# Kernel tuning notes

Hardware: AMD Instinct MI355X
Metric: run time of the kernel (lower is better)

## Reference

```python
import jax, jax.numpy as jnp
import numpy as np

WS = 4            # window_size
C = 192           # dim
NH = 6            # num_heads
HD = C // NH      # head_dim
HID = 384         # mlp hidden = int(dim * mlp_ratio)
EPS = 1e-5


def _rel_pos_index(ws):
    coords = np.stack(np.meshgrid(np.arange(ws), np.arange(ws), np.arange(ws), indexing='ij'))  # [3,ws,ws,ws]
    cf = coords.reshape(3, -1)                                # [3, N]
    rel = cf[:, :, None] - cf[:, None, :]                     # [3, N, N]
    rel = rel.transpose(1, 2, 0)                              # [N, N, 3]
    rel += ws - 1
    rel[:, :, 0] *= (2 * ws - 1) * (2 * ws - 1)
    rel[:, :, 1] *= 2 * ws - 1
    return jnp.asarray(rel.sum(-1), dtype=jnp.int32)          # [N, N]

REL_IDX = _rel_pos_index(WS)


def setup_inputs() -> dict:
    key = jax.random.key(0)
    ks = jax.random.split(key, 20)
    s = 0.02
    B, Dd, Hh, Ww = 2, 48, 48, 48
    L = Dd * Hh * Ww
    tbl = (2 * WS - 1) ** 3
    return {
        'x': jax.random.normal(ks[0], (B, L, C), jnp.float32),
        'D': Dd, 'H': Hh, 'W': Ww,
        'ln1_g': jnp.ones((C,), jnp.float32), 'ln1_b': jnp.zeros((C,), jnp.float32),
        'ln2_g': jnp.ones((C,), jnp.float32), 'ln2_b': jnp.zeros((C,), jnp.float32),
        'qkv_w': jax.random.normal(ks[1], (C, 3 * C), jnp.float32) * s,
        'qkv_b': jnp.zeros((3 * C,), jnp.float32),
        'rpb_table': jax.random.normal(ks[2], (tbl, NH), jnp.float32) * s,
        'proj_w': jax.random.normal(ks[3], (C, C), jnp.float32) * s,
        'proj_b': jnp.zeros((C,), jnp.float32),
        'fc1_w': jax.random.normal(ks[4], (C, HID), jnp.float32) * s,
        'fc1_b': jnp.zeros((HID,), jnp.float32),
        'dw_w': jax.random.normal(ks[5], (HID, 1, 3, 3, 3), jnp.float32) * s,
        'dw_b': jnp.zeros((HID,), jnp.float32),
        'bn_g': jnp.ones((HID,), jnp.float32), 'bn_b': jnp.zeros((HID,), jnp.float32),
        'bn_mean': jnp.zeros((HID,), jnp.float32), 'bn_var': jnp.ones((HID,), jnp.float32),
        'fc2_w': jax.random.normal(ks[6], (HID, C), jnp.float32) * s,
        'fc2_b': jnp.zeros((C,), jnp.float32),
    }


def _ln(x, g, b):
    m = jnp.mean(x, -1, keepdims=True)
    v = jnp.mean((x - m) ** 2, -1, keepdims=True)
    return (x - m) * jax.lax.rsqrt(v + EPS) * g + b


def _window_attn(xw, qkv_w, qkv_b, rpb_table, proj_w, proj_b):
    # xw: [nW, N, C]
    nW, N, _ = xw.shape
    qkv = (xw @ qkv_w + qkv_b).reshape(nW, N, 3, NH, HD)
    q, k, v = qkv[:, :, 0], qkv[:, :, 1], qkv[:, :, 2]   # [nW, N, NH, HD]
    scale = HD ** -0.5
    attn = jnp.einsum('wnhd,wmhd->whnm', q * scale, k)    # [nW, NH, N, N]
    bias = rpb_table[REL_IDX]                              # [N, N, NH]
    attn = attn + jnp.transpose(bias, (2, 0, 1))[None]
    attn = jax.nn.softmax(attn, axis=-1)
    out = jnp.einsum('whnm,wmhd->wnhd', attn, v).reshape(nW, N, C)
    return out @ proj_w + proj_b


def reference(x, D, H, W, ln1_g, ln1_b, ln2_g, ln2_b, qkv_w, qkv_b, rpb_table,
              proj_w, proj_b, fc1_w, fc1_b, dw_w, dw_b, bn_g, bn_b, bn_mean,
              bn_var, fc2_w, fc2_b):
    B, L, _ = x.shape
    shortcut = x
    # --- windowed attention ---
    xs = _ln(x, ln1_g, ln1_b).reshape(B, D, H, W, C)
    # D,H,W divisible by WS -> no padding
    xs = xs.reshape(B, D // WS, WS, H // WS, WS, W // WS, WS, C)
    xw = jnp.transpose(xs, (0, 1, 3, 5, 2, 4, 6, 7)).reshape(-1, WS ** 3, C)
    aw = _window_attn(xw, qkv_w, qkv_b, rpb_table, proj_w, proj_b)
    aw = aw.reshape(B, D // WS, H // WS, W // WS, WS, WS, WS, C)
    xr = jnp.transpose(aw, (0, 1, 4, 2, 5, 3, 6, 7)).reshape(B, L, C)
    x = shortcut + xr
    # --- efficient MLP: fc1 -> dwconv3d -> BN(eval) -> GELU -> fc2 ---
    y = _ln(x, ln2_g, ln2_b)
    h = y @ fc1_w + fc1_b                                  # [B, L, HID]
    hs = jnp.transpose(h, (0, 2, 1)).reshape(B, HID, D, H, W)
    hs = jax.lax.conv_general_dilated(
        hs, dw_w, window_strides=(1, 1, 1), padding='SAME',
        feature_group_count=HID,
        dimension_numbers=('NCDHW', 'OIDHW', 'NCDHW')) + dw_b[None, :, None, None, None]
    hs = (hs - bn_mean[None, :, None, None, None]) * jax.lax.rsqrt(
        bn_var[None, :, None, None, None] + EPS) * bn_g[None, :, None, None, None] + bn_b[None, :, None, None, None]
    h = jnp.transpose(hs.reshape(B, HID, L), (0, 2, 1))
    h = jax.nn.gelu(h, approximate=False)
    return x + (h @ fc2_w + fc2_b)
```

## Files before the change

kernel.cpp:

```cpp
#include <hip/hip_runtime.h>

typedef __bf16 bf16;
typedef __bf16 bf16x8 __attribute__((ext_vector_type(8)));
typedef float f32x4 __attribute__((ext_vector_type(4)));

#define L_TOT 110592
#define TOKS  221184
#define NWIN  3456

static __device__ __forceinline__ f32x4 mfma16(bf16x8 a, bf16x8 b, f32x4 c) {
    return __builtin_amdgcn_mfma_f32_16x16x32_bf16(a, b, c, 0, 0, 0);
}
static __device__ __forceinline__ bf16x8 ld8(const bf16* p) { return *(const bf16x8*)p; }

__global__ void wt_frag(const float* __restrict__ src, bf16* __restrict__ dst, int K, int N) {
    int i = blockIdx.x * 256 + threadIdx.x;
    if (i >= K * N) return;
    int kw = i & 31, col = (i >> 5) & 63, rest = i >> 11;
    int nks = K >> 5;
    int ks = rest % nks, chunk = rest / nks;
    int n = chunk * 64 + col, k = ks * 32 + kw;
    dst[i] = (bf16)src[k * N + n];
}

__global__ void bias6_build(const float* __restrict__ rpb, float* __restrict__ bias6) {
    int i = blockIdx.x * 256 + threadIdx.x;
    if (i >= 6 * 64 * 64) return;
    int h = i >> 12, n = (i >> 6) & 63, m = i & 63;
    int r0 = (n >> 4) - (m >> 4) + 3;
    int r1 = ((n >> 2) & 3) - ((m >> 2) & 3) + 3;
    int r2 = (n & 3) - (m & 3) + 3;
    bias6[i] = rpb[(r0 * 49 + r1 * 7 + r2) * 6 + h];
}

__global__ void ln1_window(const float* __restrict__ x, const float* __restrict__ g,
                           const float* __restrict__ bt, bf16* __restrict__ xw) {
    int wave = threadIdx.x >> 6, lane = threadIdx.x & 63;
    int t = blockIdx.x * 4 + wave;
    const float* row = x + (long)t * 192;
    float v0 = row[lane], v1 = row[lane + 64], v2 = row[lane + 128];
    float s = v0 + v1 + v2;
    #pragma unroll
    for (int m = 1; m < 64; m <<= 1) s += __shfl_xor(s, m);
    float mu = s * (1.0f / 192.0f);
    float d0 = v0 - mu, d1 = v1 - mu, d2 = v2 - mu;
    float q = d0 * d0 + d1 * d1 + d2 * d2;
    #pragma unroll
    for (int m = 1; m < 64; m <<= 1) q += __shfl_xor(q, m);
    float r = rsqrtf(q * (1.0f / 192.0f) + 1e-5f);
    int b = t / L_TOT, l = t - b * L_TOT;
    int dz = l / 2304, rem = l - dz * 2304;
    int hy = rem / 48, wx = rem - hy * 48;
    int w = ((b * 12 + (dz >> 2)) * 12 + (hy >> 2)) * 12 + (wx >> 2);
    int n = (dz & 3) * 16 + (hy & 3) * 4 + (wx & 3);
    bf16* o = xw + (long)w * 12288 + (lane >> 5) * 2048 + n * 32 + (lane & 31);
    o[0]    = (bf16)(d0 * r * g[lane]       + bt[lane]);
    o[4096] = (bf16)(d1 * r * g[lane + 64]  + bt[lane + 64]);
    o[8192] = (bf16)(d2 * r * g[lane + 128] + bt[lane + 128]);
}

__global__ void ln2_kernel(const bf16* __restrict__ in, const float* __restrict__ g,
                           const float* __restrict__ bt, bf16* __restrict__ y) {
    int wave = threadIdx.x >> 6, lane = threadIdx.x & 63;
    long t = blockIdx.x * 4 + wave;
    const bf16* row = in + t * 192;
    float v0 = (float)row[lane], v1 = (float)row[lane + 64], v2 = (float)row[lane + 128];
    float s = v0 + v1 + v2;
    #pragma unroll
    for (int m = 1; m < 64; m <<= 1) s += __shfl_xor(s, m);
    float mu = s * (1.0f / 192.0f);
    float d0 = v0 - mu, d1 = v1 - mu, d2 = v2 - mu;
    float q = d0 * d0 + d1 * d1 + d2 * d2;
    #pragma unroll
    for (int m = 1; m < 64; m <<= 1) q += __shfl_xor(q, m);
    float r = rsqrtf(q * (1.0f / 192.0f) + 1e-5f);
    bf16* o = y + (t >> 6) * 12288 + (lane >> 5) * 2048 + (t & 63) * 32 + (lane & 31);
    o[0]    = (bf16)(d0 * r * g[lane]       + bt[lane]);
    o[4096] = (bf16)(d1 * r * g[lane + 64]  + bt[lane + 64]);
    o[8192] = (bf16)(d2 * r * g[lane + 128] + bt[lane + 128]);
}

__global__ __launch_bounds__(256) void gemm_qkv(
    const bf16* __restrict__ xw, const bf16* __restrict__ wt,
    const float* __restrict__ bqkv,
    bf16* __restrict__ qb, bf16* __restrict__ kb_, bf16* __restrict__ vtb) {
    int m0 = blockIdx.x * 128;
    int w0 = m0 >> 6;
    int wid = threadIdx.x >> 6, lane = threadIdx.x & 63;
    int wr = wid >> 1, wc = wid & 1;
    int lo = lane & 15, hi = lane >> 4;
    f32x4 zf = {0.f, 0.f, 0.f, 0.f};

    const bf16* Ab = xw + (long)(w0 + wr) * 12288 + (lo * 32 + hi * 8);
    bf16x8 a[4][6];
    #pragma unroll
    for (int ti = 0; ti < 4; ++ti)
        #pragma unroll
        for (int ks = 0; ks < 6; ++ks)
            a[ti][ks] = ld8(Ab + ks * 2048 + ti * 512);

    #pragma unroll
    for (int nc = 0; nc < 9; ++nc) {
        int sect = nc / 3;
        int cb0 = (nc - sect * 3) * 64;
        f32x4 acc[4][2];
        #pragma unroll
        for (int i = 0; i < 4; ++i) { acc[i][0] = zf; acc[i][1] = zf; }
        const bf16* Bb = wt + (long)nc * 12288 + (wc * 32 + lo) * 32 + hi * 8;
        #pragma unroll
        for (int ks = 0; ks < 6; ++ks) {
            bf16x8 b0 = ld8(Bb + ks * 2048);
            bf16x8 b1 = ld8(Bb + ks * 2048 + 512);
            #pragma unroll
            for (int ti = 0; ti < 4; ++ti) {
                acc[ti][0] = mfma16(a[ti][ks], b0, acc[ti][0]);
                acc[ti][1] = mfma16(a[ti][ks], b1, acc[ti][1]);
            }
        }
        #pragma unroll
        for (int ti = 0; ti < 4; ++ti)
            #pragma unroll
            for (int j = 0; j < 4; ++j) {
                int trow = m0 + wr * 64 + ti * 16 + hi * 4 + j;
                int w = trow >> 6, n = trow & 63;
                #pragma unroll
                for (int tj = 0; tj < 2; ++tj) {
                    int cw = cb0 + wc * 32 + tj * 16 + lo;
                    int h = cw >> 5, d = cw & 31;
                    float val = acc[ti][tj][j] + bqkv[sect * 192 + cw];
                    long wh = (long)(w * 6 + h);
                    if (sect == 0)       qb[(wh * 64 + n) * 32 + d] = (bf16)(val * 0.17677669529663687f);
                    else if (sect == 1)  kb_[(wh * 64 + n) * 32 + d] = (bf16)val;
                    else                 vtb[(wh * 32 + d) * 64 + n] = (bf16)val;
                }
            }
    }
}

__global__ __launch_bounds__(384) void attn_light(
    const bf16* __restrict__ qb, const bf16* __restrict__ kb_,
    const bf16* __restrict__ vtb, const float* __restrict__ bias6,
    bf16* __restrict__ aw) {
    __shared__ char p_smem[6 * 8192];
    int w = blockIdx.x;
    int h = threadIdx.x >> 6;
    int lane = threadIdx.x & 63;
    int lo = lane & 15, hi = lane >> 4;
    char* ph = p_smem + h * 8192;
    long wh = (long)(w * 6 + h);
    f32x4 zf = {0.f, 0.f, 0.f, 0.f};

    bf16x8 qa[4], kb[4];
    #pragma unroll
    for (int ti = 0; ti < 4; ++ti) qa[ti] = ld8(qb  + (wh * 64 + ti * 16 + lo) * 32 + hi * 8);
    #pragma unroll
    for (int tj = 0; tj < 4; ++tj) kb[tj] = ld8(kb_ + (wh * 64 + tj * 16 + lo) * 32 + hi * 8);
    f32x4 s[4][4];
    #pragma unroll
    for (int ti = 0; ti < 4; ++ti)
        #pragma unroll
        for (int tj = 0; tj < 4; ++tj)
            s[ti][tj] = mfma16(qa[ti], kb[tj], zf);

    const float* bh = bias6 + h * 4096;
    #pragma unroll
    for (int ti = 0; ti < 4; ++ti)
        #pragma unroll
        for (int j = 0; j < 4; ++j) {
            int rr = ti * 16 + hi * 4 + j;
            float ev[4];
            #pragma unroll
            for (int tj = 0; tj < 4; ++tj) s[ti][tj][j] += bh[rr * 64 + tj * 16 + lo];
            float mx = fmaxf(fmaxf(s[ti][0][j], s[ti][1][j]), fmaxf(s[ti][2][j], s[ti][3][j]));
            #pragma unroll
            for (int m = 1; m < 16; m <<= 1) mx = fmaxf(mx, __shfl_xor(mx, m));
            float sum = 0.f;
            #pragma unroll
            for (int tj = 0; tj < 4; ++tj) { ev[tj] = __expf(s[ti][tj][j] - mx); sum += ev[tj]; }
            #pragma unroll
            for (int m = 1; m < 16; m <<= 1) sum += __shfl_xor(sum, m);
            float inv = 1.0f / sum;
            #pragma unroll
            for (int tj = 0; tj < 4; ++tj) {
                int byte = ((rr * 64 + tj * 16 + lo) * 2) ^ ((rr & 7) << 4);
                *(bf16*)(ph + byte) = (bf16)(ev[tj] * inv);
            }
        }

    f32x4 o[4][2];
    #pragma unroll
    for (int i = 0; i < 4; ++i) { o[i][0] = zf; o[i][1] = zf; }
    #pragma unroll
    for (int ks2 = 0; ks2 < 2; ++ks2) {
        bf16x8 pa[4], vb[2];
        #pragma unroll
        for (int ti = 0; ti < 4; ++ti) {
            int row = ti * 16 + lo;
            pa[ti] = *(const bf16x8*)(ph + ((row * 128 + ks2 * 64 + hi * 16) ^ ((row & 7) << 4)));
        }
        #pragma unroll
        for (int td = 0; td < 2; ++td)
            vb[td] = ld8(vtb + (wh * 32 + td * 16 + lo) * 64 + ks2 * 32 + hi * 8);
        #pragma unroll
        for (int ti = 0; ti < 4; ++ti)
            #pragma unroll
            for (int td = 0; td < 2; ++td)
                o[ti][td] = mfma16(pa[ti], vb[td], o[ti][td]);
    }
    bf16* orow = aw + wh * 2048;
    #pragma unroll
    for (int ti = 0; ti < 4; ++ti)
        #pragma unroll
        for (int td = 0; td < 2; ++td)
            #pragma unroll
            for (int j = 0; j < 4; ++j)
                orow[(ti * 16 + hi * 4 + j) * 32 + td * 16 + lo] = (bf16)o[ti][td][j];
}

__global__ __launch_bounds__(256) void gemm_proj(
    const bf16* __restrict__ aw, const bf16* __restrict__ wt,
    const float* __restrict__ bias, const float* __restrict__ x,
    bf16* __restrict__ out1) {
    int m0 = blockIdx.x * 128;
    int w0 = m0 >> 6;
    int wid = threadIdx.x >> 6, lane = threadIdx.x & 63;
    int wr = wid >> 1, wc = wid & 1;
    int lo = lane & 15, hi = lane >> 4;
    f32x4 zf = {0.f, 0.f, 0.f, 0.f};

    const bf16* Ab = aw + (long)(w0 + wr) * 12288 + (lo * 32 + hi * 8);
    bf16x8 a[4][6];
    #pragma unroll
    for (int ti = 0; ti < 4; ++ti)
        #pragma unroll
        for (int ks = 0; ks < 6; ++ks)
            a[ti][ks] = ld8(Ab + ks * 2048 + ti * 512);

    #pragma unroll
    for (int nc = 0; nc < 3; ++nc) {
        f32x4 acc[4][2];
        #pragma unroll
        for (int i = 0; i < 4; ++i) { acc[i][0] = zf; acc[i][1] = zf; }
        const bf16* Bb = wt + (long)nc * 12288 + (wc * 32 + lo) * 32 + hi * 8;
        #pragma unroll
        for (int ks = 0; ks < 6; ++ks) {
            bf16x8 b0 = ld8(Bb + ks * 2048);
            bf16x8 b1 = ld8(Bb + ks * 2048 + 512);
            #pragma unroll
            for (int ti = 0; ti < 4; ++ti) {
                acc[ti][0] = mfma16(a[ti][ks], b0, acc[ti][0]);
                acc[ti][1] = mfma16(a[ti][ks], b1, acc[ti][1]);
            }
        }
        #pragma unroll
        for (int ti = 0; ti < 4; ++ti)
            #pragma unroll
            for (int j = 0; j < 4; ++j) {
                int trow = m0 + wr * 64 + ti * 16 + hi * 4 + j;
                int wv = trow >> 6, n = trow & 63;
                int bb = wv / 1728; int rem = wv - bb * 1728;
                int dq = rem / 144; int rem2 = rem - dq * 144;
                int hq = rem2 / 12; int wq = rem2 - hq * 12;
                int l = (dq * 4 + (n >> 4)) * 2304 + (hq * 4 + ((n >> 2) & 3)) * 48 + (wq * 4 + (n & 3));
                long base = ((long)bb * L_TOT + l) * 192;
                #pragma unroll
                for (int tj = 0; tj < 2; ++tj) {
                    int col = nc * 64 + wc * 32 + tj * 16 + lo;
                    out1[base + col] = (bf16)(x[base + col] + acc[ti][tj][j] + bias[col]);
                }
            }
    }
}

__global__ __launch_bounds__(256) void gemm_fc1(
    const bf16* __restrict__ y, const bf16* __restrict__ wt,
    const float* __restrict__ bias, bf16* __restrict__ h_t) {
    __shared__ bf16 tl[64][136];
    int m0 = blockIdx.x * 128;
    int c0 = m0 >> 6;
    int wid = threadIdx.x >> 6, lane = threadIdx.x & 63;
    int wr = wid >> 1, wc = wid & 1;
    int lo = lane & 15, hi = lane >> 4;
    f32x4 zf = {0.f, 0.f, 0.f, 0.f};
    int bb = m0 / L_TOT; int l0 = m0 - bb * L_TOT;
    int col = threadIdx.x >> 2, seg = threadIdx.x & 3;

    const bf16* Ab = y + (long)(c0 + wr) * 12288 + (lo * 32 + hi * 8);
    bf16x8 a[4][6];
    #pragma unroll
    for (int ti = 0; ti < 4; ++ti)
        #pragma unroll
        for (int ks = 0; ks < 6; ++ks)
            a[ti][ks] = ld8(Ab + ks * 2048 + ti * 512);

    #pragma unroll
    for (int nc = 0; nc < 6; ++nc) {
        f32x4 acc[4][2];
        #pragma unroll
        for (int i = 0; i < 4; ++i) { acc[i][0] = zf; acc[i][1] = zf; }
        const bf16* Bb = wt + (long)nc * 12288 + (wc * 32 + lo) * 32 + hi * 8;
        #pragma unroll
        for (int ks = 0; ks < 6; ++ks) {
            bf16x8 b0 = ld8(Bb + ks * 2048);
            bf16x8 b1 = ld8(Bb + ks * 2048 + 512);
            #pragma unroll
            for (int ti = 0; ti < 4; ++ti) {
                acc[ti][0] = mfma16(a[ti][ks], b0, acc[ti][0]);
                acc[ti][1] = mfma16(a[ti][ks], b1, acc[ti][1]);
            }
        }
        if (nc) __syncthreads();
        #pragma unroll
        for (int ti = 0; ti < 4; ++ti)
            #pragma unroll
            for (int tj = 0; tj < 2; ++tj)
                #pragma unroll
                for (int j = 0; j < 4; ++j) {
                    int rl = wr * 64 + ti * 16 + hi * 4 + j;
                    int cl = wc * 32 + tj * 16 + lo;
                    tl[cl][rl] = (bf16)(acc[ti][tj][j] + bias[nc * 64 + cl]);
                }
        __syncthreads();
        bf16* dst = h_t + ((long)bb * 384 + nc * 64 + col) * L_TOT + l0 + seg * 32;
        #pragma unroll
        for (int i8 = 0; i8 < 4; ++i8)
            *(bf16x8*)(dst + i8 * 8) = *(const bf16x8*)(&tl[col][seg * 32 + i8 * 8]);
    }
}

__global__ __launch_bounds__(320) void dwconv_bn_gelu(
    const bf16* __restrict__ h_t, const float* __restrict__ wconv,
    const float* __restrict__ cb, const float* __restrict__ bng,
    const float* __restrict__ bnb, const float* __restrict__ bnm,
    const float* __restrict__ bnv, bf16* __restrict__ g_t) {
    __shared__ __align__(16) bf16 tile[289 * 56];
    int blk = blockIdx.x;
    int bb = blk / 4608; int rem = blk - bb * 4608;
    int ch = rem / 12; int zb = rem - ch * 12; int z0 = zb * 4;
    const bf16* src = h_t + ((long)bb * 384 + ch) * L_TOT;

    int y = threadIdx.x / 6, cx = threadIdx.x - y * 6, x0 = cx * 8;
    bool active = threadIdx.x < 288;

    uint4 zv = make_uint4(0u, 0u, 0u, 0u);
    for (int i = threadIdx.x; i < 295; i += 320) {
        int e = (i < 7) ? i * 8 : ((i - 7 + 1) * 56 + 48);
        *(uint4*)(tile + e) = zv;
    }
    if (active) {
        #pragma unroll
        for (int zi = 0; zi < 6; ++zi) {
            int gz = z0 - 1 + zi;
            uint4 val = zv;
            if (gz >= 0 && gz < 48) val = *(const uint4*)(src + (long)gz * 2304 + y * 48 + x0);
            *(uint4*)(tile + (1 + zi * 48 + y) * 56 + x0) = val;
        }
    }
    float wgt[27];
    #pragma unroll
    for (int i = 0; i < 27; ++i) wgt[i] = wconv[ch * 27 + i];
    float scale = bng[ch] * rsqrtf(bnv[ch] + 1e-5f);
    float shift = bnb[ch] - bnm[ch] * scale;
    float cbias = cb[ch];
    __syncthreads();

    if (active) {
        __builtin_assume(y < 48);
        bool up_ok = (y > 0), dn_ok = (y < 47);
        bf16* dstc = g_t + ((long)bb * 384 + ch) * L_TOT + (long)z0 * 2304 + y * 48 + x0;
        float acc[4][8];
        #pragma unroll
        for (int p = 0; p < 4; ++p)
            #pragma unroll
            for (int k = 0; k < 8; ++k) acc[p][k] = 0.f;

        #pragma unroll
        for (int zi = 0; zi < 6; ++zi) {
            const bf16* plane = tile + (1 + zi * 48) * 56;
            #pragma unroll
            for (int dy = 0; dy < 3; ++dy) {
                bool ok = (dy == 1) || (dy == 0 ? up_ok : dn_ok);
                if (ok) {
                    const bf16* rp = plane + (y + dy - 1) * 56 + x0;
                    bf16x8 mv = ld8(rp);
                    float s[10];
                    s[0] = (float)rp[-1];
                    #pragma unroll
                    for (int i = 0; i < 8; ++i) s[i + 1] = (float)mv[i];
                    s[9] = (float)rp[8];
                    #pragma unroll
                    for (int dz = 0; dz < 3; ++dz) {
                        int p = zi - dz;
                        if (p >= 0 && p <= 3) {
                            float w0 = wgt[dz * 9 + dy * 3 + 0];
                            float w1 = wgt[dz * 9 + dy * 3 + 1];
                            float w2 = wgt[dz * 9 + dy * 3 + 2];
                            #pragma unroll
                            for (int k = 0; k < 8; ++k)
                                acc[p][k] = fmaf(w0, s[k], fmaf(w1, s[k + 1], fmaf(w2, s[k + 2], acc[p][k])));
                        }
                    }
                }
            }
            if (zi >= 2) {
                int p = zi - 2;
                bf16x8 ov;
                #pragma unroll
                for (int k = 0; k < 8; ++k) {
                    float v = acc[p][k] + cbias;
                    v = fmaf(v, scale, shift);
                    float v2 = v * v;
                    float u2 = v * fmaf(v2, 0.10294357f, 2.3022080918f);
                    float e  = exp2f(u2);
                    float q  = __builtin_amdgcn_rcpf(e + 1.0f);
                    ov[k] = (bf16)(v - v * q);
                }
                *(bf16x8*)(dstc + p * 2304) = ov;
            }
        }
    }
}

__global__ __launch_bounds__(256) void gemm_fc2(
    const bf16* __restrict__ g_t, const bf16* __restrict__ wt,
    const float* __restrict__ bias, const bf16* __restrict__ out1,
    float* __restrict__ out) {
    __shared__ bf16 As[2][4096];
    int m0 = blockIdx.x * 64;
    int wc = threadIdx.x >> 6, lane = threadIdx.x & 63;
    int lo = lane & 15, hi = lane >> 4;
    int bb = m0 / L_TOT, l0 = m0 - bb * L_TOT;
    f32x4 zf = {0.f, 0.f, 0.f, 0.f};
    f32x4 acc[3][4];
    #pragma unroll
    for (int tj = 0; tj < 3; ++tj)
        #pragma unroll
        for (int ti = 0; ti < 4; ++ti) acc[tj][ti] = zf;

    int sch = threadIdx.x >> 3;
    int seg = threadIdx.x & 7;
    const bf16* srcb = g_t + ((long)bb * 384 + sch) * L_TOT + l0 + seg * 8;

    bf16x8 r[2][2];
    #pragma unroll
    for (int p = 0; p < 2; ++p) r[0][p] = ld8(srcb + (long)(p * 32) * L_TOT);
    #pragma unroll
    for (int p = 0; p < 2; ++p)
        #pragma unroll
        for (int i = 0; i < 8; ++i)
            As[0][(seg * 8 + i) * 64 + ((p * 32 + sch) ^ (((seg ^ i) & 7) << 3))] = r[0][p][i];
    #pragma unroll
    for (int p = 0; p < 2; ++p) r[0][p] = ld8(srcb + (long)(64 + p * 32) * L_TOT);
    #pragma unroll
    for (int p = 0; p < 2; ++p) r[1][p] = ld8(srcb + (long)(128 + p * 32) * L_TOT);

    float res[3][4][4];
    #pragma unroll
    for (int tj = 0; tj < 3; ++tj)
        #pragma unroll
        for (int ti = 0; ti < 4; ++ti)
            #pragma unroll
            for (int j = 0; j < 4; ++j) {
                long trow = m0 + ti * 16 + hi * 4 + j;
                res[tj][ti][j] = (float)out1[trow * 192 + wc * 48 + tj * 16 + lo];
            }
    __syncthreads();

    #pragma unroll
    for (int t = 0; t < 6; ++t) {
        const bf16* Ac = As[t & 1];
        #pragma unroll
        for (int ksin = 0; ksin < 2; ++ksin) {
            bf16x8 a[4];
            #pragma unroll
            for (int ti = 0; ti < 4; ++ti) {
                int rr = ti * 16 + lo;
                int S = ((rr >> 3) ^ rr) & 7;
                a[ti] = *(const bf16x8*)&Ac[rr * 64 + ((ksin * 32 + hi * 8) ^ (S << 3))];
            }
            #pragma unroll
            for (int tj = 0; tj < 3; ++tj) {
                int cstart = wc * 48 + tj * 16;
                bf16x8 b0 = ld8(wt + ((long)((cstart >> 6) * 12 + t * 2 + ksin) * 64 + (cstart & 63) + lo) * 32 + hi * 8);
                #pragma unroll
                for (int ti = 0; ti < 4; ++ti)
                    acc[tj][ti] = mfma16(a[ti], b0, acc[tj][ti]);
            }
        }
        if (t < 5) {
            bf16* An = As[(t + 1) & 1];
            #pragma unroll
            for (int p = 0; p < 2; ++p)
                #pragma unroll
                for (int i = 0; i < 8; ++i)
                    An[(seg * 8 + i) * 64 + ((p * 32 + sch) ^ (((seg ^ i) & 7) << 3))] = r[t & 1][p][i];
        }
        if (t < 3) {
            #pragma unroll
            for (int p = 0; p < 2; ++p)
                r[t & 1][p] = ld8(srcb + (long)((t + 3) * 64 + p * 32) * L_TOT);
        }
        __syncthreads();
    }
    #pragma unroll
    for (int tj = 0; tj < 3; ++tj)
        #pragma unroll
        for (int ti = 0; ti < 4; ++ti)
            #pragma unroll
            for (int j = 0; j < 4; ++j) {
                long trow = m0 + ti * 16 + hi * 4 + j;
                int col = wc * 48 + tj * 16 + lo;
                out[trow * 192 + col] = res[tj][ti][j] + acc[tj][ti][j] + bias[col];
            }
}

extern "C" void kernel_launch(void* const* d_in, const int* in_sizes, int n_in,
                              void* d_out, int out_size, void* d_ws, size_t ws_size,
                              hipStream_t stream) {
    (void)in_sizes; (void)n_in; (void)out_size; (void)ws_size;
    const float* x     = (const float*)d_in[0];
    const float* ln1g  = (const float*)d_in[4];
    const float* ln1b  = (const float*)d_in[5];
    const float* ln2g  = (const float*)d_in[6];
    const float* ln2b  = (const float*)d_in[7];
    const float* qkvw  = (const float*)d_in[8];
    const float* qkvb  = (const float*)d_in[9];
    const float* rpb   = (const float*)d_in[10];
    const float* projw = (const float*)d_in[11];
    const float* projb = (const float*)d_in[12];
    const float* fc1w  = (const float*)d_in[13];
    const float* fc1b  = (const float*)d_in[14];
    const float* dww   = (const float*)d_in[15];
    const float* dwb   = (const float*)d_in[16];
    const float* bng   = (const float*)d_in[17];
    const float* bnb   = (const float*)d_in[18];
    const float* bnm   = (const float*)d_in[19];
    const float* bnv   = (const float*)d_in[20];
    const float* fc2w  = (const float*)d_in[21];
    const float* fc2b  = (const float*)d_in[22];
    float* out = (float*)d_out;

    char* ws = (char*)d_ws;
    size_t o = 0;
    bf16*  out1 = (bf16*)(ws + o);
    bf16*  vt_buf = (bf16*)(ws + o + 84934656); o += 169869312;
    bf16*  h_t  = (bf16*)(ws + o); o += 169869312;
    bf16*  region1 = (bf16*)(ws + o); o += 169869312;
    bf16*  xw  = region1;
    bf16*  aw  = region1 + 42467328;
    bf16*  yb  = region1;
    bf16*  g_t = region1;
    bf16*  qkvwt  = (bf16*)(ws + o); o += 221184;
    bf16*  projwt = (bf16*)(ws + o); o += 73728;
    bf16*  fc1wt  = (bf16*)(ws + o); o += 147456;
    bf16*  fc2wt  = (bf16*)(ws + o); o += 147456;
    float* bias6  = (float*)(ws + o); o += 98304;

    bf16* q_buf  = h_t;
    bf16* k_buf  = h_t + 42467328;

    wt_frag<<<(110592 + 255) / 256, 256, 0, stream>>>(qkvw, qkvwt, 192, 576);
    wt_frag<<<(36864 + 255) / 256, 256, 0, stream>>>(projw, projwt, 192, 192);
    wt_frag<<<(73728 + 255) / 256, 256, 0, stream>>>(fc1w, fc1wt, 192, 384);
    wt_frag<<<(73728 + 255) / 256, 256, 0, stream>>>(fc2w, fc2wt, 384, 192);
    bias6_build<<<96, 256, 0, stream>>>(rpb, bias6);

    ln1_window<<<55296, 256, 0, stream>>>(x, ln1g, ln1b, xw);
    gemm_qkv<<<1728, 256, 0, stream>>>(xw, qkvwt, qkvb, q_buf, k_buf, vt_buf);
    attn_light<<<NWIN, 384, 0, stream>>>(q_buf, k_buf, vt_buf, bias6, aw);
    gemm_proj<<<1728, 256, 0, stream>>>(aw, projwt, projb, x, out1);
    ln2_kernel<<<55296, 256, 0, stream>>>(out1, ln2g, ln2b, yb);
    gemm_fc1<<<1728, 256, 0, stream>>>(yb, fc1wt, fc1b, h_t);
    dwconv_bn_gelu<<<9216, 320, 0, stream>>>(h_t, dww, dwb, bng, bnb, bnm, bnv, g_t);
    gemm_fc2<<<3456, 256, 0, stream>>>(g_t, fc2wt, fc2b, out1, out);
}
```

Baseline: 741.2 us.

## Fuse LayerNorm2 into fc1 GEMM by storing residual in fragment layout

The proj GEMM now writes the residual out1 directly in the tiled fragment layout that fc1 consumes. LayerNorm2 is computed inside gemm_fc1 on the register-resident A fragments using cross-lane shuffles, and the standalone ln2 kernel is removed. This saves one full read and write pass over the activation tensor plus a kernel launch. The costs are a one-pass variance formula (E[x^2]-mu^2), which is less numerically robust, and scattered residual reads in fc2 that must follow the new layout.

```diff
diff --git a/kernel.cpp b/kernel.cpp
--- a/kernel.cpp
+++ b/kernel.cpp
@@ -54,27 +54,6 @@
     int w = ((b * 12 + (dz >> 2)) * 12 + (hy >> 2)) * 12 + (wx >> 2);
     int n = (dz & 3) * 16 + (hy & 3) * 4 + (wx & 3);
     bf16* o = xw + (long)w * 12288 + (lane >> 5) * 2048 + n * 32 + (lane & 31);
-    o[0]    = (bf16)(d0 * r * g[lane]       + bt[lane]);
-    o[4096] = (bf16)(d1 * r * g[lane + 64]  + bt[lane + 64]);
-    o[8192] = (bf16)(d2 * r * g[lane + 128] + bt[lane + 128]);
-}
-
-__global__ void ln2_kernel(const bf16* __restrict__ in, const float* __restrict__ g,
-                           const float* __restrict__ bt, bf16* __restrict__ y) {
-    int wave = threadIdx.x >> 6, lane = threadIdx.x & 63;
-    long t = blockIdx.x * 4 + wave;
-    const bf16* row = in + t * 192;
-    float v0 = (float)row[lane], v1 = (float)row[lane + 64], v2 = (float)row[lane + 128];
-    float s = v0 + v1 + v2;
-    #pragma unroll
-    for (int m = 1; m < 64; m <<= 1) s += __shfl_xor(s, m);
-    float mu = s * (1.0f / 192.0f);
-    float d0 = v0 - mu, d1 = v1 - mu, d2 = v2 - mu;
-    float q = d0 * d0 + d1 * d1 + d2 * d2;
-    #pragma unroll
-    for (int m = 1; m < 64; m <<= 1) q += __shfl_xor(q, m);
-    float r = rsqrtf(q * (1.0f / 192.0f) + 1e-5f);
-    bf16* o = y + (t >> 6) * 12288 + (lane >> 5) * 2048 + (t & 63) * 32 + (lane & 31);
     o[0]    = (bf16)(d0 * r * g[lane]       + bt[lane]);
     o[4096] = (bf16)(d1 * r * g[lane + 64]  + bt[lane + 64]);
     o[8192] = (bf16)(d2 * r * g[lane + 128] + bt[lane + 128]);
@@ -262,19 +241,23 @@
                 int dq = rem / 144; int rem2 = rem - dq * 144;
                 int hq = rem2 / 12; int wq = rem2 - hq * 12;
                 int l = (dq * 4 + (n >> 4)) * 2304 + (hq * 4 + ((n >> 2) & 3)) * 48 + (wq * 4 + (n & 3));
-                long base = ((long)bb * L_TOT + l) * 192;
+                long t = (long)bb * L_TOT + l;
+                long fbase = (t >> 6) * 12288 + (t & 63) * 32;
+                long xbase = t * 192;
                 #pragma unroll
                 for (int tj = 0; tj < 2; ++tj) {
                     int col = nc * 64 + wc * 32 + tj * 16 + lo;
-                    out1[base + col] = (bf16)(x[base + col] + acc[ti][tj][j] + bias[col]);
+                    float val = x[xbase + col] + acc[ti][tj][j] + bias[col];
+                    out1[fbase + (nc * 2 + wc) * 2048 + tj * 16 + lo] = (bf16)val;
                 }
             }
     }
 }
 
 __global__ __launch_bounds__(256) void gemm_fc1(
-    const bf16* __restrict__ y, const bf16* __restrict__ wt,
-    const float* __restrict__ bias, bf16* __restrict__ h_t) {
+    const bf16* __restrict__ o1, const bf16* __restrict__ wt,
+    const float* __restrict__ bias, const float* __restrict__ g2,
+    const float* __restrict__ b2, bf16* __restrict__ h_t) {
     __shared__ bf16 tl[64][136];
     int m0 = blockIdx.x * 128;
     int c0 = m0 >> 6;
@@ -285,13 +268,50 @@
     int bb = m0 / L_TOT; int l0 = m0 - bb * L_TOT;
     int col = threadIdx.x >> 2, seg = threadIdx.x & 3;
 
-    const bf16* Ab = y + (long)(c0 + wr) * 12288 + (lo * 32 + hi * 8);
+    const bf16* Ab = o1 + (long)(c0 + wr) * 12288 + (lo * 32 + hi * 8);
     bf16x8 a[4][6];
     #pragma unroll
     for (int ti = 0; ti < 4; ++ti)
         #pragma unroll
         for (int ks = 0; ks < 6; ++ks)
             a[ti][ks] = ld8(Ab + ks * 2048 + ti * 512);
+
+    #pragma unroll
+    for (int ti = 0; ti < 4; ++ti) {
+        float sum = 0.f, sq = 0.f;
+        #pragma unroll
+        for (int ks = 0; ks < 6; ++ks)
+            #pragma unroll
+            for (int i = 0; i < 8; ++i) {
+                float v = (float)a[ti][ks][i];
+                sum += v;
+                sq = fmaf(v, v, sq);
+            }
+        sum += __shfl_xor(sum, 16); sum += __shfl_xor(sum, 32);
+        sq  += __shfl_xor(sq, 16);  sq  += __shfl_xor(sq, 32);
+        float mu = sum * (1.0f / 192.0f);
+        float var = sq * (1.0f / 192.0f) - mu * mu;
+        float r = rsqrtf(var + 1e-5f);
+        #pragma unroll
+        for (int ks = 0; ks < 6; ++ks) {
+            const float* gp = g2 + ks * 32 + hi * 8;
+            const float* bp = b2 + ks * 32 + hi * 8;
+            f32x4 g0 = *(const f32x4*)gp, g1 = *(const f32x4*)(gp + 4);
+            f32x4 bv0 = *(const f32x4*)bp, bv1 = *(const f32x4*)(bp + 4);
+            bf16x8 an;
+            #pragma unroll
+            for (int i = 0; i < 4; ++i) {
+                float v = (float)a[ti][ks][i];
+                an[i] = (bf16)((v - mu) * r * g0[i] + bv0[i]);
+            }
+            #pragma unroll
+            for (int i = 0; i < 4; ++i) {
+                float v = (float)a[ti][ks][4 + i];
+                an[4 + i] = (bf16)((v - mu) * r * g1[i] + bv1[i]);
+            }
+            a[ti][ks] = an;
+        }
+    }
 
     #pragma unroll
     for (int nc = 0; nc < 6; ++nc) {
@@ -454,6 +474,7 @@
     #pragma unroll
     for (int p = 0; p < 2; ++p) r[1][p] = ld8(srcb + (long)(128 + p * 32) * L_TOT);
 
+    long fbase = (long)(m0 >> 6) * 12288;
     float res[3][4][4];
     #pragma unroll
     for (int tj = 0; tj < 3; ++tj)
@@ -461,8 +482,9 @@
         for (int ti = 0; ti < 4; ++ti)
             #pragma unroll
             for (int j = 0; j < 4; ++j) {
-                long trow = m0 + ti * 16 + hi * 4 + j;
-                res[tj][ti][j] = (float)out1[trow * 192 + wc * 48 + tj * 16 + lo];
+                int trow6 = ti * 16 + hi * 4 + j;
+                int c = wc * 48 + tj * 16 + lo;
+                res[tj][ti][j] = (float)out1[fbase + (c >> 5) * 2048 + trow6 * 32 + (c & 31)];
             }
     __syncthreads();
 
@@ -548,7 +570,6 @@
     bf16*  region1 = (bf16*)(ws + o); o += 169869312;
     bf16*  xw  = region1;
     bf16*  aw  = region1 + 42467328;
-    bf16*  yb  = region1;
     bf16*  g_t = region1;
     bf16*  qkvwt  = (bf16*)(ws + o); o += 221184;
     bf16*  projwt = (bf16*)(ws + o); o += 73728;
@@ -569,8 +590,7 @@
     gemm_qkv<<<1728, 256, 0, stream>>>(xw, qkvwt, qkvb, q_buf, k_buf, vt_buf);
     attn_light<<<NWIN, 384, 0, stream>>>(q_buf, k_buf, vt_buf, bias6, aw);
     gemm_proj<<<1728, 256, 0, stream>>>(aw, projwt, projb, x, out1);
-    ln2_kernel<<<55296, 256, 0, stream>>>(out1, ln2g, ln2b, yb);
-    gemm_fc1<<<1728, 256, 0, stream>>>(yb, fc1wt, fc1b, h_t);
+    gemm_fc1<<<1728, 256, 0, stream>>>(out1, fc1wt, fc1b, ln2g, ln2b, h_t);
     dwconv_bn_gelu<<<9216, 320, 0, stream>>>(h_t, dww, dwb, bng, bnb, bnm, bnv, g_t);
     gemm_fc2<<<3456, 256, 0, stream>>>(g_t, fc2wt, fc2b, out1, out);
 }
```

After: 765.9 us. +3.3%, slower.

## Fuse LayerNorm2 into projection GEMM epilogue with per-window blocks

Applied to the files above, without the earlier changes.

Replaces the separate proj GEMM and LN2 kernels with one kernel. Each block computes a whole 64-token window across all 192 columns. Row sums and sums of squares are reduced across the four waves through shared memory, and the block writes both the residual (out1) and the normalized bf16 activations. out1 moves to the same fragment-tiled layout the GEMMs use, and fc2's residual read is updated to match. This removes one full read/write pass over the activation tensor and one launch. The cost is a single-pass E[x^2]-mu^2 variance, which is less numerically robust, and a weight reload per block.

```diff
diff --git a/kernel.cpp b/kernel.cpp
--- a/kernel.cpp
+++ b/kernel.cpp
@@ -54,27 +54,6 @@
     int w = ((b * 12 + (dz >> 2)) * 12 + (hy >> 2)) * 12 + (wx >> 2);
     int n = (dz & 3) * 16 + (hy & 3) * 4 + (wx & 3);
     bf16* o = xw + (long)w * 12288 + (lane >> 5) * 2048 + n * 32 + (lane & 31);
-    o[0]    = (bf16)(d0 * r * g[lane]       + bt[lane]);
-    o[4096] = (bf16)(d1 * r * g[lane + 64]  + bt[lane + 64]);
-    o[8192] = (bf16)(d2 * r * g[lane + 128] + bt[lane + 128]);
-}
-
-__global__ void ln2_kernel(const bf16* __restrict__ in, const float* __restrict__ g,
-                           const float* __restrict__ bt, bf16* __restrict__ y) {
-    int wave = threadIdx.x >> 6, lane = threadIdx.x & 63;
-    long t = blockIdx.x * 4 + wave;
-    const bf16* row = in + t * 192;
-    float v0 = (float)row[lane], v1 = (float)row[lane + 64], v2 = (float)row[lane + 128];
-    float s = v0 + v1 + v2;
-    #pragma unroll
-    for (int m = 1; m < 64; m <<= 1) s += __shfl_xor(s, m);
-    float mu = s * (1.0f / 192.0f);
-    float d0 = v0 - mu, d1 = v1 - mu, d2 = v2 - mu;
-    float q = d0 * d0 + d1 * d1 + d2 * d2;
-    #pragma unroll
-    for (int m = 1; m < 64; m <<= 1) q += __shfl_xor(q, m);
-    float r = rsqrtf(q * (1.0f / 192.0f) + 1e-5f);
-    bf16* o = y + (t >> 6) * 12288 + (lane >> 5) * 2048 + (t & 63) * 32 + (lane & 31);
     o[0]    = (bf16)(d0 * r * g[lane]       + bt[lane]);
     o[4096] = (bf16)(d1 * r * g[lane + 64]  + bt[lane + 64]);
     o[8192] = (bf16)(d2 * r * g[lane + 128] + bt[lane + 128]);
@@ -217,59 +196,98 @@
                 orow[(ti * 16 + hi * 4 + j) * 32 + td * 16 + lo] = (bf16)o[ti][td][j];
 }
 
-__global__ __launch_bounds__(256) void gemm_proj(
+__global__ __launch_bounds__(256) void gemm_proj_ln(
     const bf16* __restrict__ aw, const bf16* __restrict__ wt,
     const float* __restrict__ bias, const float* __restrict__ x,
-    bf16* __restrict__ out1) {
-    int m0 = blockIdx.x * 128;
-    int w0 = m0 >> 6;
-    int wid = threadIdx.x >> 6, lane = threadIdx.x & 63;
-    int wr = wid >> 1, wc = wid & 1;
+    const float* __restrict__ g2, const float* __restrict__ b2,
+    bf16* __restrict__ out1, bf16* __restrict__ y) {
+    __shared__ float sred[64][4][2];
+    int w0 = blockIdx.x;
+    int wc = threadIdx.x >> 6, lane = threadIdx.x & 63;
     int lo = lane & 15, hi = lane >> 4;
     f32x4 zf = {0.f, 0.f, 0.f, 0.f};
-
-    const bf16* Ab = aw + (long)(w0 + wr) * 12288 + (lo * 32 + hi * 8);
-    bf16x8 a[4][6];
-    #pragma unroll
-    for (int ti = 0; ti < 4; ++ti)
-        #pragma unroll
-        for (int ks = 0; ks < 6; ++ks)
-            a[ti][ks] = ld8(Ab + ks * 2048 + ti * 512);
-
-    #pragma unroll
-    for (int nc = 0; nc < 3; ++nc) {
-        f32x4 acc[4][2];
-        #pragma unroll
-        for (int i = 0; i < 4; ++i) { acc[i][0] = zf; acc[i][1] = zf; }
-        const bf16* Bb = wt + (long)nc * 12288 + (wc * 32 + lo) * 32 + hi * 8;
-        #pragma unroll
-        for (int ks = 0; ks < 6; ++ks) {
-            bf16x8 b0 = ld8(Bb + ks * 2048);
-            bf16x8 b1 = ld8(Bb + ks * 2048 + 512);
-            #pragma unroll
-            for (int ti = 0; ti < 4; ++ti) {
-                acc[ti][0] = mfma16(a[ti][ks], b0, acc[ti][0]);
-                acc[ti][1] = mfma16(a[ti][ks], b1, acc[ti][1]);
-            }
-        }
+    f32x4 acc[3][4];
+    #pragma unroll
+    for (int tj = 0; tj < 3; ++tj)
+        #pragma unroll
+        for (int ti = 0; ti < 4; ++ti) acc[tj][ti] = zf;
+
+    const bf16* Ab = aw + (long)w0 * 12288 + lo * 32 + hi * 8;
+    #pragma unroll
+    for (int ks = 0; ks < 6; ++ks) {
+        bf16x8 a[4];
+        #pragma unroll
+        for (int ti = 0; ti < 4; ++ti) a[ti] = ld8(Ab + ks * 2048 + ti * 512);
+        #pragma unroll
+        for (int tj = 0; tj < 3; ++tj) {
+            int col0 = wc * 48 + tj * 16;
+            bf16x8 b0 = ld8(wt + ((long)((col0 >> 6) * 6 + ks) * 64 + (col0 & 63) + lo) * 32 + hi * 8);
+            #pragma unroll
+            for (int ti = 0; ti < 4; ++ti)
+                acc[tj][ti] = mfma16(a[ti], b0, acc[tj][ti]);
+        }
+    }
+
+    int bb = w0 / 1728; int remw = w0 - bb * 1728;
+    int dq = remw / 144; int rem2 = remw - dq * 144;
+    int hq = rem2 / 12; int wq = rem2 - hq * 12;
+
+    int lcache[4][4];
+    float sum[4][4], sq[4][4];
+    #pragma unroll
+    for (int ti = 0; ti < 4; ++ti)
+        #pragma unroll
+        for (int j = 0; j < 4; ++j) {
+            int n = ti * 16 + hi * 4 + j;
+            int l = (dq * 4 + (n >> 4)) * 2304 + (hq * 4 + ((n >> 2) & 3)) * 48 + (wq * 4 + (n & 3));
+            lcache[ti][j] = l;
+            long xbase = ((long)bb * L_TOT + l) * 192;
+            float s = 0.f, q = 0.f;
+            #pragma unroll
+            for (int tj = 0; tj < 3; ++tj) {
+                int col = wc * 48 + tj * 16 + lo;
+                float v = x[xbase + col] + acc[tj][ti][j] + bias[col];
+                acc[tj][ti][j] = v;
+                s += v; q = fmaf(v, v, q);
+            }
+            #pragma unroll
+            for (int m = 1; m < 16; m <<= 1) { s += __shfl_xor(s, m); q += __shfl_xor(q, m); }
+            sum[ti][j] = s; sq[ti][j] = q;
+        }
+    if (lo == 0) {
         #pragma unroll
         for (int ti = 0; ti < 4; ++ti)
             #pragma unroll
             for (int j = 0; j < 4; ++j) {
-                int trow = m0 + wr * 64 + ti * 16 + hi * 4 + j;
-                int wv = trow >> 6, n = trow & 63;
-                int bb = wv / 1728; int rem = wv - bb * 1728;
-                int dq = rem / 144; int rem2 = rem - dq * 144;
-                int hq = rem2 / 12; int wq = rem2 - hq * 12;
-                int l = (dq * 4 + (n >> 4)) * 2304 + (hq * 4 + ((n >> 2) & 3)) * 48 + (wq * 4 + (n & 3));
-                long base = ((long)bb * L_TOT + l) * 192;
-                #pragma unroll
-                for (int tj = 0; tj < 2; ++tj) {
-                    int col = nc * 64 + wc * 32 + tj * 16 + lo;
-                    out1[base + col] = (bf16)(x[base + col] + acc[ti][tj][j] + bias[col]);
-                }
-            }
-    }
+                int rr = ti * 16 + hi * 4 + j;
+                sred[rr][wc][0] = sum[ti][j];
+                sred[rr][wc][1] = sq[ti][j];
+            }
+    }
+    __syncthreads();
+
+    #pragma unroll
+    for (int ti = 0; ti < 4; ++ti)
+        #pragma unroll
+        for (int j = 0; j < 4; ++j) {
+            int rr = ti * 16 + hi * 4 + j;
+            float S = sred[rr][0][0] + sred[rr][1][0] + sred[rr][2][0] + sred[rr][3][0];
+            float Q = sred[rr][0][1] + sred[rr][1][1] + sred[rr][2][1] + sred[rr][3][1];
+            float mu = S * (1.0f / 192.0f);
+            float var = Q * (1.0f / 192.0f) - mu * mu;
+            float r = rsqrtf(var + 1e-5f);
+            long t = (long)bb * L_TOT + lcache[ti][j];
+            long fb = (t >> 6) * 12288 + (t & 63) * 32;
+            #pragma unroll
+            for (int tj = 0; tj < 3; ++tj) {
+                int col0 = wc * 48 + tj * 16;
+                int col = col0 + lo;
+                float v = acc[tj][ti][j];
+                long idx = fb + (col0 >> 5) * 2048 + (col0 & 31) + lo;
+                out1[idx] = (bf16)v;
+                y[idx]    = (bf16)((v - mu) * r * g2[col] + b2[col]);
+            }
+        }
 }
 
 __global__ __launch_bounds__(256) void gemm_fc1(
@@ -454,6 +472,7 @@
     #pragma unroll
     for (int p = 0; p < 2; ++p) r[1][p] = ld8(srcb + (long)(128 + p * 32) * L_TOT);
 
+    long fbase = (long)(m0 >> 6) * 12288;
     float res[3][4][4];
     #pragma unroll
     for (int tj = 0; tj < 3; ++tj)
@@ -461,8 +480,9 @@
         for (int ti = 0; ti < 4; ++ti)
             #pragma unroll
             for (int j = 0; j < 4; ++j) {
-                long trow = m0 + ti * 16 + hi * 4 + j;
-                res[tj][ti][j] = (float)out1[trow * 192 + wc * 48 + tj * 16 + lo];
+                int trow6 = ti * 16 + hi * 4 + j;
+                int c = wc * 48 + tj * 16 + lo;
+                res[tj][ti][j] = (float)out1[fbase + (c >> 5) * 2048 + trow6 * 32 + (c & 31)];
             }
     __syncthreads();
 
@@ -547,8 +567,8 @@
     bf16*  h_t  = (bf16*)(ws + o); o += 169869312;
     bf16*  region1 = (bf16*)(ws + o); o += 169869312;
     bf16*  xw  = region1;
+    bf16*  yb  = region1;
     bf16*  aw  = region1 + 42467328;
-    bf16*  yb  = region1;
     bf16*  g_t = region1;
     bf16*  qkvwt  = (bf16*)(ws + o); o += 221184;
     bf16*  projwt = (bf16*)(ws + o); o += 73728;
@@ -568,8 +588,7 @@
     ln1_window<<<55296, 256, 0, stream>>>(x, ln1g, ln1b, xw);
     gemm_qkv<<<1728, 256, 0, stream>>>(xw, qkvwt, qkvb, q_buf, k_buf, vt_buf);
     attn_light<<<NWIN, 384, 0, stream>>>(q_buf, k_buf, vt_buf, bias6, aw);
-    gemm_proj<<<1728, 256, 0, stream>>>(aw, projwt, projb, x, out1);
-    ln2_kernel<<<55296, 256, 0, stream>>>(out1, ln2g, ln2b, yb);
+    gemm_proj_ln<<<NWIN, 256, 0, stream>>>(aw, projwt, projb, x, ln2g, ln2b, out1, yb);
     gemm_fc1<<<1728, 256, 0, stream>>>(yb, fc1wt, fc1b, h_t);
     dwconv_bn_gelu<<<9216, 320, 0, stream>>>(h_t, dww, dwb, bng, bnb, bnm, bnv, g_t);
     gemm_fc2<<<3456, 256, 0, stream>>>(g_t, fc2wt, fc2b, out1, out);
```

Measured after the change: 787.5 us. 1.06x slower.
